# Kernel tuning notes

Hardware: AMD Instinct MI355X
Metric: run time of the kernel (lower is better)

The kernel has to match this reference:

```python
import jax, jax.numpy as jnp
import numpy as np

H = 128

def _gru_cell(x, h, w_ih, w_hh, b_ih, b_hh):
    # PyTorch GRUCell semantics; w_* are [3H, H], gate order r, z, n.
    gi = x @ w_ih.T + b_ih
    gh = h @ w_hh.T + b_hh
    ir, iz, in_ = jnp.split(gi, 3, axis=-1)
    hr, hz, hn = jnp.split(gh, 3, axis=-1)
    r = jax.nn.sigmoid(ir + hr)
    z = jax.nn.sigmoid(iz + hz)
    n = jnp.tanh(in_ + r * hn)
    return (1.0 - z) * n + z * h


def setup_inputs() -> dict:
    key = jax.random.key(0)
    ks = jax.random.split(key, 24)
    s = 0.05
    d = {}
    d["weapon_features"] = jax.random.normal(ks[0], (4, 8, 64, 4), jnp.float32)
    d["target_features"] = jax.random.normal(ks[1], (4, 8, 64, 4), jnp.float32)
    d["edge_features"] = jax.random.uniform(ks[2], (4, 8, 64, 64, 1), jnp.float32)
    # projections (torch Linear convention: weight [out, in])
    d["wp_w"] = jax.random.normal(ks[3], (H, 4), jnp.float32) * s
    d["wp_b"] = jnp.zeros((H,), jnp.float32)
    d["tp_w"] = jax.random.normal(ks[4], (H, 4), jnp.float32) * s
    d["tp_b"] = jnp.zeros((H,), jnp.float32)
    d["ep_w"] = jax.random.normal(ks[5], (H, 1), jnp.float32) * s
    d["ep_b"] = jnp.zeros((H,), jnp.float32)
    # message / edge-update linears [H, 3H]
    d["eu_w"] = jax.random.normal(ks[6], (H, 3 * H), jnp.float32) * s
    d["eu_b"] = jnp.zeros((H,), jnp.float32)
    d["wm_w"] = jax.random.normal(ks[7], (H, 3 * H), jnp.float32) * s
    d["wm_b"] = jnp.zeros((H,), jnp.float32)
    d["tm_w"] = jax.random.normal(ks[8], (H, 3 * H), jnp.float32) * s
    d["tm_b"] = jnp.zeros((H,), jnp.float32)
    # GRU cells
    d["gru_w_ih_w"] = jax.random.normal(ks[9], (3 * H, H), jnp.float32) * s
    d["gru_w_hh_w"] = jax.random.normal(ks[10], (3 * H, H), jnp.float32) * s
    d["gru_b_ih_w"] = jnp.zeros((3 * H,), jnp.float32)
    d["gru_b_hh_w"] = jnp.zeros((3 * H,), jnp.float32)
    d["gru_w_ih_t"] = jax.random.normal(ks[11], (3 * H, H), jnp.float32) * s
    d["gru_w_hh_t"] = jax.random.normal(ks[12], (3 * H, H), jnp.float32) * s
    d["gru_b_ih_t"] = jnp.zeros((3 * H,), jnp.float32)
    d["gru_b_hh_t"] = jnp.zeros((3 * H,), jnp.float32)
    return d


def reference(weapon_features, target_features, edge_features,
              wp_w, wp_b, tp_w, tp_b, ep_w, ep_b,
              eu_w, eu_b, wm_w, wm_b, tm_w, tm_b,
              gru_w_ih_w, gru_w_hh_w, gru_b_ih_w, gru_b_hh_w,
              gru_w_ih_t, gru_w_hh_t, gru_b_ih_t, gru_b_hh_t):
    B, P, W = weapon_features.shape[:3]
    T = target_features.shape[2]
    h = wp_w.shape[0]

    weapon_h = weapon_features @ wp_w.T + wp_b          # [B,P,W,H]
    target_h = target_features @ tp_w.T + tp_b          # [B,P,T,H]
    edge_h = edge_features @ ep_w.T + ep_b              # [B,P,W,T,H]

    # edge_update(cat([w_exp, t_exp, edge_h])) == sum of three slice-linears,
    # broadcast-added; avoids materializing the [B,P,W,T,3H] concat.
    ea, eb, ec = eu_w[:, :h], eu_w[:, h:2 * h], eu_w[:, 2 * h:]
    edge_pre = ((weapon_h @ ea.T)[:, :, :, None, :]
                + (target_h @ eb.T)[:, :, None, :, :]
                + edge_h @ ec.T + eu_b)
    edge_h_new = jnp.tanh(edge_pre)                     # [B,P,W,T,H]

    # weapon_msg(cat([w_exp, t_exp, edge_h_new])).sum(dim=3)
    wa, wb, wc = wm_w[:, :h], wm_w[:, h:2 * h], wm_w[:, 2 * h:]
    weapon_msgs = (T * (weapon_h @ wa.T)
                   + (target_h.sum(axis=2) @ wb.T)[:, :, None, :]
                   + edge_h_new.sum(axis=3) @ wc.T
                   + T * wm_b)                          # [B,P,W,H]

    # target_msg(cat([t_exp, w_exp, edge_h_new])).sum(dim=2)
    ta, tb, tc = tm_w[:, :h], tm_w[:, h:2 * h], tm_w[:, 2 * h:]
    target_msgs = (W * (target_h @ ta.T)
                   + (weapon_h.sum(axis=2) @ tb.T)[:, :, None, :]
                   + edge_h_new.sum(axis=2) @ tc.T
                   + W * tm_b)                          # [B,P,T,H]

    weapon_h_new = _gru_cell(weapon_msgs.reshape(-1, h), weapon_h.reshape(-1, h),
                             gru_w_ih_w, gru_w_hh_w, gru_b_ih_w, gru_b_hh_w)
    weapon_h_new = weapon_h_new.reshape(B, P, W, h)

    target_h_new = _gru_cell(target_msgs.reshape(-1, h), target_h.reshape(-1, h),
                             gru_w_ih_t, gru_w_hh_t, gru_b_ih_t, gru_b_hh_t)
    target_h_new = target_h_new.reshape(B, P, T, h)

    return weapon_h_new, target_h_new, edge_h_new
```

## Files before the change

### kernel.cpp

```cpp
#include <hip/hip_runtime.h>

#define DEV __device__ __forceinline__

constexpr int H  = 128;
constexpr int BP = 32;
constexpr int NR = 2048;

constexpr int WH_OFF    = 0;
constexpr int TH_OFF    = WH_OFF + NR*H;
constexpr int WHS_OFF   = TH_OFF + NR*H;
constexpr int THS_OFF   = WHS_OFF + BP*H;
constexpr int V1_OFF    = THS_OFF + BP*H;
constexpr int C0_OFF    = V1_OFF + H;
constexpr int WT1_OFF   = C0_OFF + H;
constexpr int WT2_OFF   = WT1_OFF + 128*640;
constexpr int WCT_OFF   = WT2_OFF + 128*640;
constexpr int TCT_OFF   = WCT_OFF + 128*128;
constexpr int WIHWT_OFF = TCT_OFF + 128*128;
constexpr int WIHTT_OFF = WIHWT_OFF + 128*384;
constexpr int WBT_OFF   = WIHTT_OFF + 128*384;
constexpr int TBT_OFF   = WBT_OFF + 128*128;
constexpr int OUT1_OFF  = TBT_OFF + 128*128;
constexpr int OUT2_OFF  = OUT1_OFF + NR*640;
constexpr int ESW_OFF   = OUT2_OFF + NR*640;
constexpr int ESTP_OFF  = ESW_OFF + NR*H;
constexpr int MSGW_OFF  = ESTP_OFF + 8*NR*H;
constexpr int MSGT_OFF  = MSGW_OFF + NR*H;
constexpr int GIW_OFF   = MSGT_OFF + NR*H;
constexpr int GIT_OFF   = GIW_OFF + NR*384;
constexpr int WBV_OFF   = GIT_OFF + NR*384;
constexpr int TBV_OFF   = WBV_OFF + BP*H;

DEV float fast_tanh(float x) {
  float e = __builtin_amdgcn_exp2f(x * 2.8853900817779268f);
  return fmaf(-2.0f, __builtin_amdgcn_rcpf(e + 1.0f), 1.0f);
}
DEV float fast_sigmoid(float x) {
  float e = __builtin_amdgcn_exp2f(x * -1.4426950408889634f);
  return __builtin_amdgcn_rcpf(1.0f + e);
}

__global__ __launch_bounds__(256) void k1_proj_transpose(
    const float* __restrict__ wf, const float* __restrict__ tf,
    const float* __restrict__ wp_w, const float* __restrict__ wp_b,
    const float* __restrict__ tp_w, const float* __restrict__ tp_b,
    const float* __restrict__ eu_w, const float* __restrict__ wm_w,
    const float* __restrict__ tm_w,
    const float* __restrict__ whh_w, const float* __restrict__ whh_t,
    const float* __restrict__ wih_w, const float* __restrict__ wih_t,
    float* __restrict__ ws)
{
  int bid = blockIdx.x, tid = threadIdx.x;
  if (bid < 2048) {
    int gid = bid*256 + tid;
    int m = gid >> 7;
    int j = gid & 127;
    int side = m >> 11;
    int n = m & 2047;
    const float* F  = side ? tf : wf;
    const float* Pw = side ? tp_w : wp_w;
    const float* Pb = side ? tp_b : wp_b;
    float4 x  = *(const float4*)&F[n*4];
    float4 wv = *(const float4*)&Pw[j*4];
    float v = x.x*wv.x + x.y*wv.y + x.z*wv.z + x.w*wv.w + Pb[j];
    ws[(side ? TH_OFF : WH_OFF) + n*H + j] = v;
  } else {
    int idx = (bid - 2048)*256 + tid;
    if (idx < 131072) {
      int which = idx >> 14;
      int r = idx & 16383;
      int k = r >> 7, j = r & 127;
      float v; float* dst;
      switch (which) {
        case 0: v = eu_w[j*384 + k];        dst = ws + WT1_OFF + k*640 + j;       break;
        case 1: v = wm_w[j*384 + k];        dst = ws + WT1_OFF + k*640 + 128 + j; break;
        case 2: v = eu_w[j*384 + 128 + k];  dst = ws + WT2_OFF + k*640 + j;       break;
        case 3: v = tm_w[j*384 + k];        dst = ws + WT2_OFF + k*640 + 128 + j; break;
        case 4: v = wm_w[j*384 + 256 + k];  dst = ws + WCT_OFF + k*128 + j;       break;
        case 5: v = tm_w[j*384 + 256 + k];  dst = ws + TCT_OFF + k*128 + j;       break;
        case 6: v = wm_w[j*384 + 128 + k];  dst = ws + WBT_OFF + k*128 + j;       break;
        default:v = tm_w[j*384 + 128 + k];  dst = ws + TBT_OFF + k*128 + j;       break;
      }
      *dst = v;
    } else {
      int idx2 = idx - 131072;
      int which = idx2 / 49152;
      int r = idx2 % 49152;
      int k = r / 384, j = r % 384;
      float v; float* dst;
      switch (which) {
        case 0: v = whh_w[j*128 + k]; dst = ws + WT1_OFF + k*640 + 256 + j; break;
        case 1: v = whh_t[j*128 + k]; dst = ws + WT2_OFF + k*640 + 256 + j; break;
        case 2: v = wih_w[j*128 + k]; dst = ws + WIHWT_OFF + k*384 + j;     break;
        default:v = wih_t[j*128 + k]; dst = ws + WIHTT_OFF + k*384 + j;     break;
      }
      *dst = v;
    }
  }
}

__global__ __launch_bounds__(256) void k2_sums(
    float* __restrict__ ws,
    const float* __restrict__ ep_w, const float* __restrict__ ep_b,
    const float* __restrict__ eu_w, const float* __restrict__ eu_b)
{
  int bid = blockIdx.x, tid = threadIdx.x;
  if (bid < 32) {
    int j = tid & 127, half = tid >> 7;
    const float* src = ws + (half ? TH_OFF : WH_OFF) + bid*64*H + j;
    float s = 0.f;
    #pragma unroll 8
    for (int t = 0; t < 64; ++t) s += src[t*H];
    ws[(half ? THS_OFF : WHS_OFF) + bid*H + j] = s;
  } else if (tid < 128) {
    int j = tid;
    float s1 = 0.f, s0 = 0.f;
    for (int k = 0; k < 128; ++k) {
      float ec = eu_w[j*384 + 256 + k];
      s1 = fmaf(ec, ep_w[k], s1);
      s0 = fmaf(ec, ep_b[k], s0);
    }
    ws[V1_OFF + j] = s1;
    ws[C0_OFF + j] = s0 + eu_b[j];
  }
}

#define FMA4(A, s, Wv) do { A.x = fmaf(s, Wv.x, A.x); A.y = fmaf(s, Wv.y, A.y); \
                            A.z = fmaf(s, Wv.z, A.z); A.w = fmaf(s, Wv.w, A.w); } while (0)

DEV void stage_x_direct(float* Xs, const float* __restrict__ X, int row0, int tid) {
  const float* src = X + row0*128;
  #pragma unroll
  for (int q = 0; q < 4; ++q) {
    int idx = q*1024 + tid*4;
    *(float4*)&Xs[idx] = *(const float4*)&src[idx];
  }
}

DEV void stage_x_sum8(float* Xs, const float* __restrict__ base, int row0, int tid) {
  #pragma unroll
  for (int q = 0; q < 4; ++q) {
    int idx = q*1024 + tid*4;
    float4 s = *(const float4*)&base[row0*128 + idx];
    #pragma unroll
    for (int wt = 1; wt < 8; ++wt) {
      float4 v = *(const float4*)&base[wt*(NR*H) + row0*128 + idx];
      s.x += v.x; s.y += v.y; s.z += v.z; s.w += v.w;
    }
    *(float4*)&Xs[idx] = s;
  }
}

DEV void gemm_core(const float* __restrict__ Wt, int ldw, int j0,
                   const float* Xs, float* Ws, int tid, float4 acc[4])
{
  const int tc = tid & 31, tr = tid >> 5;
  const int jj = tc*4, r0 = tr*4;
  #pragma unroll
  for (int i = 0; i < 4; ++i) acc[i] = make_float4(0.f, 0.f, 0.f, 0.f);
  for (int kc = 0; kc < 128; kc += 32) {
    __syncthreads();
    #pragma unroll
    for (int q = 0; q < 4; ++q) {
      int idx = q*1024 + tid*4;
      int kk = idx >> 7, j = idx & 127;
      *(float4*)&Ws[idx] = *(const float4*)&Wt[(kc+kk)*ldw + j0 + j];
    }
    __syncthreads();
    #pragma unroll
    for (int kk = 0; kk < 32; kk += 4) {
      float4 w0 = *(const float4*)&Ws[(kk+0)*128 + jj];
      float4 w1 = *(const float4*)&Ws[(kk+1)*128 + jj];
      float4 w2 = *(const float4*)&Ws[(kk+2)*128 + jj];
      float4 w3 = *(const float4*)&Ws[(kk+3)*128 + jj];
      #pragma unroll
      for (int rr = 0; rr < 4; ++rr) {
        float4 xq = *(const float4*)&Xs[(r0+rr)*128 + kc + kk];
        FMA4(acc[rr], xq.x, w0);
        FMA4(acc[rr], xq.y, w1);
        FMA4(acc[rr], xq.z, w2);
        FMA4(acc[rr], xq.w, w3);
      }
    }
  }
}

__global__ __launch_bounds__(256) void k3_gemm1(float* __restrict__ ws)
{
  __shared__ float Xs[32*128];
  __shared__ float Wsh[32*128];
  int bid = blockIdx.x, tid = threadIdx.x;
  const int tc = tid & 31, tr = tid >> 5;
  const int jj = tc*4, r0 = tr*4;
  float4 acc[4];
  if (bid < 640) {
    int side = bid >= 320;
    int b2 = bid - (side ? 320 : 0);
    int rt = b2 & 63, ct = b2 >> 6;
    int row0 = rt*32;
    stage_x_direct(Xs, ws + (side ? TH_OFF : WH_OFF), row0, tid);
    gemm_core(ws + (side ? WT2_OFF : WT1_OFF), 640, ct*128, Xs, Wsh, tid, acc);
    float* C = ws + (side ? OUT2_OFF : OUT1_OFF);
    #pragma unroll
    for (int rr = 0; rr < 4; ++rr)
      *(float4*)&C[(row0+r0+rr)*640 + ct*128 + jj] = acc[rr];
  } else {
    int which = bid - 640;
    stage_x_direct(Xs, ws + (which ? WHS_OFF : THS_OFF), 0, tid);
    gemm_core(ws + (which ? TBT_OFF : WBT_OFF), 128, 0, Xs, Wsh, tid, acc);
    float* C = ws + (which ? TBV_OFF : WBV_OFF);
    #pragma unroll
    for (int rr = 0; rr < 4; ++rr)
      *(float4*)&C[(r0+rr)*128 + jj] = acc[rr];
  }
}

__global__ __launch_bounds__(256) void k4_edge(
    const float* __restrict__ ef, float* __restrict__ ws, float* __restrict__ out)
{
  __shared__ float e_lds[8*64];
  __shared__ float red[2][8][128];
  int bid = blockIdx.x, tid = threadIdx.x;
  int bp = bid >> 3, wt = bid & 7;
  int j = tid & 127, tsel = tid >> 7;
  float v1j = ws[V1_OFF + j], c0j = ws[C0_OFF + j];
  {
    const float* esrc = ef + bp*4096 + wt*512;
    *(float2*)&e_lds[tid*2] = *(const float2*)&esrc[tid*2];
  }
  float a_reg[8];
  #pragma unroll
  for (int w = 0; w < 8; ++w)
    a_reg[w] = ws[OUT1_OFF + (bp*64 + wt*8 + w)*640 + j];
  __syncthreads();
  float tsum[8] = {0,0,0,0,0,0,0,0};
  float* edst = out + 524288 + (bp*64 + wt*8)*64*128;
  const float* btp = ws + OUT2_OFF + bp*64*640 + j;
  float* pdst = ws + ESTP_OFF + wt*(NR*H) + bp*64*128 + j;
  for (int i = 0; i < 32; ++i) {
    int t = 2*i + tsel;
    float base = btp[t*640] + c0j;
    float wsum = 0.f;
    #pragma unroll
    for (int w = 0; w < 8; ++w) {
      float ev = e_lds[w*64 + t];
      float pre = a_reg[w] + fmaf(ev, v1j, base);
      float hv = fast_tanh(pre);
      edst[(w*64 + t)*128 + j] = hv;
      tsum[w] += hv;
      wsum += hv;
    }
    pdst[t*128] = wsum;
  }
  #pragma unroll
  for (int w = 0; w < 8; ++w) red[tsel][w][j] = tsum[w];
  __syncthreads();
  if (tsel == 0) {
    #pragma unroll
    for (int w = 0; w < 8; ++w)
      ws[ESW_OFF + (bp*64 + wt*8 + w)*128 + j] = red[0][w][j] + red[1][w][j];
  }
}

__global__ __launch_bounds__(256) void k5_gemm2(
    float* __restrict__ ws, const float* __restrict__ wm_b, const float* __restrict__ tm_b)
{
  __shared__ float Xs[32*128];
  __shared__ float Wsh[32*128];
  int bid = blockIdx.x, tid = threadIdx.x;
  int side = bid >> 6, rt = bid & 63;
  int row0 = rt*32;
  const int tc = tid & 31, tr = tid >> 5;
  const int jj = tc*4, r0 = tr*4;
  if (side == 0) stage_x_direct(Xs, ws + ESW_OFF, row0, tid);
  else           stage_x_sum8(Xs, ws + ESTP_OFF, row0, tid);
  float4 acc[4];
  gemm_core(ws + (side ? TCT_OFF : WCT_OFF), 128, 0, Xs, Wsh, tid, acc);
  const float* OUTx = ws + (side ? OUT2_OFF : OUT1_OFF);
  const float* BV   = ws + (side ? TBV_OFF : WBV_OFF);
  const float* mb   = side ? tm_b : wm_b;
  float* MSG        = ws + (side ? MSGT_OFF : MSGW_OFF);
  float4 b4 = *(const float4*)&mb[jj];
  #pragma unroll
  for (int rr = 0; rr < 4; ++rr) {
    int n = row0 + r0 + rr;
    float4 wa4 = *(const float4*)&OUTx[n*640 + 128 + jj];
    float4 bv4 = *(const float4*)&BV[(n >> 6)*128 + jj];
    float4 r;
    r.x = acc[rr].x + 64.f*wa4.x + bv4.x + 64.f*b4.x;
    r.y = acc[rr].y + 64.f*wa4.y + bv4.y + 64.f*b4.y;
    r.z = acc[rr].z + 64.f*wa4.z + bv4.z + 64.f*b4.z;
    r.w = acc[rr].w + 64.f*wa4.w + bv4.w + 64.f*b4.w;
    *(float4*)&MSG[n*128 + jj] = r;
  }
}

__global__ __launch_bounds__(256) void k6_gemm3(float* __restrict__ ws)
{
  __shared__ float Xs[32*128];
  __shared__ float Wsh[32*128];
  int bid = blockIdx.x, tid = threadIdx.x;
  int side = bid >= 192;
  int b2 = bid - (side ? 192 : 0);
  int rt = b2 & 63, ct = b2 >> 6;
  int row0 = rt*32;
  const int tc = tid & 31, tr = tid >> 5;
  const int jj = tc*4, r0 = tr*4;
  stage_x_direct(Xs, ws + (side ? MSGT_OFF : MSGW_OFF), row0, tid);
  float4 acc[4];
  gemm_core(ws + (side ? WIHTT_OFF : WIHWT_OFF), 384, ct*128, Xs, Wsh, tid, acc);
  float* C = ws + (side ? GIT_OFF : GIW_OFF);
  #pragma unroll
  for (int rr = 0; rr < 4; ++rr)
    *(float4*)&C[(row0+r0+rr)*384 + ct*128 + jj] = acc[rr];
}

__global__ __launch_bounds__(256) void k7_gru(
    const float* __restrict__ ws, float* __restrict__ out,
    const float* __restrict__ bih_w, const float* __restrict__ bhh_w,
    const float* __restrict__ bih_t, const float* __restrict__ bhh_t)
{
  int gid = blockIdx.x*256 + threadIdx.x;
  int m = gid >> 7, j = gid & 127;
  int side = m >> 11, n = m & 2047;
  const float* GI = ws + (side ? GIT_OFF : GIW_OFF) + n*384;
  const float* GH = ws + (side ? OUT2_OFF : OUT1_OFF) + n*640 + 256;
  const float* Hv = ws + (side ? TH_OFF : WH_OFF) + n*128;
  const float* bi = side ? bih_t : bih_w;
  const float* bh = side ? bhh_t : bhh_w;
  float gir = GI[j]       + bi[j];
  float giz = GI[128 + j] + bi[128 + j];
  float gin = GI[256 + j] + bi[256 + j];
  float ghr = GH[j]       + bh[j];
  float ghz = GH[128 + j] + bh[128 + j];
  float ghn = GH[256 + j] + bh[256 + j];
  float r  = fast_sigmoid(gir + ghr);
  float z  = fast_sigmoid(giz + ghz);
  float nn = fast_tanh(gin + r*ghn);
  float h  = Hv[j];
  out[side*262144 + n*128 + j] = (1.f - z)*nn + z*h;
}

extern "C" void kernel_launch(void* const* d_in, const int* in_sizes, int n_in,
                              void* d_out, int out_size, void* d_ws, size_t ws_size,
                              hipStream_t stream)
{
  const float* wf    = (const float*)d_in[0];
  const float* tf    = (const float*)d_in[1];
  const float* ef    = (const float*)d_in[2];
  const float* wp_w  = (const float*)d_in[3];
  const float* wp_b  = (const float*)d_in[4];
  const float* tp_w  = (const float*)d_in[5];
  const float* tp_b  = (const float*)d_in[6];
  const float* ep_w  = (const float*)d_in[7];
  const float* ep_b  = (const float*)d_in[8];
  const float* eu_w  = (const float*)d_in[9];
  const float* eu_b  = (const float*)d_in[10];
  const float* wm_w  = (const float*)d_in[11];
  const float* wm_b  = (const float*)d_in[12];
  const float* tm_w  = (const float*)d_in[13];
  const float* tm_b  = (const float*)d_in[14];
  const float* wih_w = (const float*)d_in[15];
  const float* whh_w = (const float*)d_in[16];
  const float* bih_w = (const float*)d_in[17];
  const float* bhh_w = (const float*)d_in[18];
  const float* wih_t = (const float*)d_in[19];
  const float* whh_t = (const float*)d_in[20];
  const float* bih_t = (const float*)d_in[21];
  const float* bhh_t = (const float*)d_in[22];
  float* ws  = (float*)d_ws;
  float* out = (float*)d_out;

  hipLaunchKernelGGL(k1_proj_transpose, dim3(3328), dim3(256), 0, stream,
                     wf, tf, wp_w, wp_b, tp_w, tp_b, eu_w, wm_w, tm_w,
                     whh_w, whh_t, wih_w, wih_t, ws);
  hipLaunchKernelGGL(k2_sums,  dim3(33),   dim3(256), 0, stream, ws, ep_w, ep_b, eu_w, eu_b);
  hipLaunchKernelGGL(k3_gemm1, dim3(642),  dim3(256), 0, stream, ws);
  hipLaunchKernelGGL(k4_edge,  dim3(256),  dim3(256), 0, stream, ef, ws, out);
  hipLaunchKernelGGL(k5_gemm2, dim3(128),  dim3(256), 0, stream, ws, wm_b, tm_b);
  hipLaunchKernelGGL(k6_gemm3, dim3(384),  dim3(256), 0, stream, ws);
  hipLaunchKernelGGL(k7_gru,   dim3(2048), dim3(256), 0, stream, ws, out,
                     bih_w, bhh_w, bih_t, bhh_t);
}
```

Before: 188.7 us.

## Split weight transpose into LDS-tiled kernel, fuse sums into projection, widen edge grid

Weight transposes move into a separate LDS-tiled kernel (20 blocks) so that global reads and writes are coalesced. The per-batch hidden sums are now computed directly from raw features in the projection kernel, which removes the k2 launch. The edge kernel splits the weapon dimension four ways instead of eight per block, doubling the grid. It stages the target projection in LDS and writes edge outputs with nontemporal stores. The price is a 16-way partial-sum buffer that k5 must reduce, plus more LDS use per edge block.

```diff
diff --git a/kernel.cpp b/kernel.cpp
--- a/kernel.cpp
+++ b/kernel.cpp
@@ -24,7 +24,7 @@
 constexpr int OUT2_OFF  = OUT1_OFF + NR*640;
 constexpr int ESW_OFF   = OUT2_OFF + NR*640;
 constexpr int ESTP_OFF  = ESW_OFF + NR*H;
-constexpr int MSGW_OFF  = ESTP_OFF + 8*NR*H;
+constexpr int MSGW_OFF  = ESTP_OFF + 16*NR*H;
 constexpr int MSGT_OFF  = MSGW_OFF + NR*H;
 constexpr int GIW_OFF   = MSGT_OFF + NR*H;
 constexpr int GIT_OFF   = GIW_OFF + NR*384;
@@ -40,16 +40,62 @@
   return __builtin_amdgcn_rcpf(1.0f + e);
 }
 
-__global__ __launch_bounds__(256) void k1_proj_transpose(
-    const float* __restrict__ wf, const float* __restrict__ tf,
-    const float* __restrict__ wp_w, const float* __restrict__ wp_b,
-    const float* __restrict__ tp_w, const float* __restrict__ tp_b,
+__global__ __launch_bounds__(256) void k0_transpose(
     const float* __restrict__ eu_w, const float* __restrict__ wm_w,
     const float* __restrict__ tm_w,
     const float* __restrict__ whh_w, const float* __restrict__ whh_t,
     const float* __restrict__ wih_w, const float* __restrict__ wih_t,
     float* __restrict__ ws)
 {
+  __shared__ float T[128*133];
+  int tt = blockIdx.x, tid = threadIdx.x;
+  const float* src; int rs = 384, co = 0, row0 = 0, dsto, ldd, j0;
+  switch (tt) {
+    case 0:  src=eu_w;  dsto=WT1_OFF; ldd=640; j0=0;   break;
+    case 1:  src=wm_w;  dsto=WT1_OFF; ldd=640; j0=128; break;
+    case 2: case 3: case 4:
+      src=whh_w; rs=128; row0=(tt-2)*128; dsto=WT1_OFF; ldd=640; j0=256+(tt-2)*128; break;
+    case 5:  src=eu_w;  co=128; dsto=WT2_OFF; ldd=640; j0=0; break;
+    case 6:  src=tm_w;  dsto=WT2_OFF; ldd=640; j0=128; break;
+    case 7: case 8: case 9:
+      src=whh_t; rs=128; row0=(tt-7)*128; dsto=WT2_OFF; ldd=640; j0=256+(tt-7)*128; break;
+    case 10: src=wm_w; co=256; dsto=WCT_OFF; ldd=128; j0=0; break;
+    case 11: src=tm_w; co=256; dsto=TCT_OFF; ldd=128; j0=0; break;
+    case 12: src=wm_w; co=128; dsto=WBT_OFF; ldd=128; j0=0; break;
+    case 13: src=tm_w; co=128; dsto=TBT_OFF; ldd=128; j0=0; break;
+    case 14: case 15: case 16:
+      src=wih_w; rs=128; row0=(tt-14)*128; dsto=WIHWT_OFF; ldd=384; j0=(tt-14)*128; break;
+    default:
+      src=wih_t; rs=128; row0=(tt-17)*128; dsto=WIHTT_OFF; ldd=384; j0=(tt-17)*128; break;
+  }
+  #pragma unroll
+  for (int q = 0; q < 16; ++q) {
+    int idx = q*1024 + tid*4;
+    int r = idx >> 7, c = idx & 127;
+    float4 v = *(const float4*)&src[(row0 + r)*rs + co + c];
+    float* t = &T[r*133 + c];
+    t[0]=v.x; t[1]=v.y; t[2]=v.z; t[3]=v.w;
+  }
+  __syncthreads();
+  float* dst = ws + dsto;
+  #pragma unroll
+  for (int q = 0; q < 64; ++q) {
+    int idx = q*256 + tid;
+    int k = idx >> 7, j = idx & 127;
+    dst[k*ldd + j0 + j] = T[j*133 + k];
+  }
+}
+
+__global__ __launch_bounds__(256) void k1_proj(
+    const float* __restrict__ wf, const float* __restrict__ tf,
+    const float* __restrict__ wp_w, const float* __restrict__ wp_b,
+    const float* __restrict__ tp_w, const float* __restrict__ tp_b,
+    const float* __restrict__ eu_w,
+    const float* __restrict__ ep_w, const float* __restrict__ ep_b,
+    const float* __restrict__ eu_b,
+    float* __restrict__ ws)
+{
+  __shared__ float fs[2][32][4];
   int bid = blockIdx.x, tid = threadIdx.x;
   if (bid < 2048) {
     int gid = bid*256 + tid;
@@ -65,63 +111,40 @@
     float v = x.x*wv.x + x.y*wv.y + x.z*wv.z + x.w*wv.w + Pb[j];
     ws[(side ? TH_OFF : WH_OFF) + n*H + j] = v;
   } else {
-    int idx = (bid - 2048)*256 + tid;
-    if (idx < 131072) {
-      int which = idx >> 14;
-      int r = idx & 16383;
-      int k = r >> 7, j = r & 127;
-      float v; float* dst;
-      switch (which) {
-        case 0: v = eu_w[j*384 + k];        dst = ws + WT1_OFF + k*640 + j;       break;
-        case 1: v = wm_w[j*384 + k];        dst = ws + WT1_OFF + k*640 + 128 + j; break;
-        case 2: v = eu_w[j*384 + 128 + k];  dst = ws + WT2_OFF + k*640 + j;       break;
-        case 3: v = tm_w[j*384 + k];        dst = ws + WT2_OFF + k*640 + 128 + j; break;
-        case 4: v = wm_w[j*384 + 256 + k];  dst = ws + WCT_OFF + k*128 + j;       break;
-        case 5: v = tm_w[j*384 + 256 + k];  dst = ws + TCT_OFF + k*128 + j;       break;
-        case 6: v = wm_w[j*384 + 128 + k];  dst = ws + WBT_OFF + k*128 + j;       break;
-        default:v = tm_w[j*384 + 128 + k];  dst = ws + TBT_OFF + k*128 + j;       break;
+    {
+      int side = tid >> 7, r = tid & 127;
+      int bp = r >> 2, c = r & 3;
+      const float* F = side ? tf : wf;
+      float s = 0.f;
+      #pragma unroll 8
+      for (int w = 0; w < 64; ++w) s += F[bp*256 + w*4 + c];
+      fs[side][bp][c] = s;
+    }
+    __syncthreads();
+    {
+      int side = tid >> 7, j = tid & 127;
+      const float* Pw = side ? tp_w : wp_w;
+      const float* Pb = side ? tp_b : wp_b;
+      float4 wv = *(const float4*)&Pw[j*4];
+      float pb = Pb[j] * 64.f;
+      float* dst = ws + (side ? THS_OFF : WHS_OFF) + j;
+      #pragma unroll 4
+      for (int bp = 0; bp < 32; ++bp) {
+        float4 f = *(const float4*)&fs[side][bp][0];
+        dst[bp*128] = f.x*wv.x + f.y*wv.y + f.z*wv.z + f.w*wv.w + pb;
       }
-      *dst = v;
-    } else {
-      int idx2 = idx - 131072;
-      int which = idx2 / 49152;
-      int r = idx2 % 49152;
-      int k = r / 384, j = r % 384;
-      float v; float* dst;
-      switch (which) {
-        case 0: v = whh_w[j*128 + k]; dst = ws + WT1_OFF + k*640 + 256 + j; break;
-        case 1: v = whh_t[j*128 + k]; dst = ws + WT2_OFF + k*640 + 256 + j; break;
-        case 2: v = wih_w[j*128 + k]; dst = ws + WIHWT_OFF + k*384 + j;     break;
-        default:v = wih_t[j*128 + k]; dst = ws + WIHTT_OFF + k*384 + j;     break;
+    }
+    if (tid < 128) {
+      int j = tid;
+      float s1 = 0.f, s0 = 0.f;
+      for (int k = 0; k < 128; ++k) {
+        float ec = eu_w[j*384 + 256 + k];
+        s1 = fmaf(ec, ep_w[k], s1);
+        s0 = fmaf(ec, ep_b[k], s0);
       }
-      *dst = v;
-    }
-  }
-}
-
-__global__ __launch_bounds__(256) void k2_sums(
-    float* __restrict__ ws,
-    const float* __restrict__ ep_w, const float* __restrict__ ep_b,
-    const float* __restrict__ eu_w, const float* __restrict__ eu_b)
-{
-  int bid = blockIdx.x, tid = threadIdx.x;
-  if (bid < 32) {
-    int j = tid & 127, half = tid >> 7;
-    const float* src = ws + (half ? TH_OFF : WH_OFF) + bid*64*H + j;
-    float s = 0.f;
-    #pragma unroll 8
-    for (int t = 0; t < 64; ++t) s += src[t*H];
-    ws[(half ? THS_OFF : WHS_OFF) + bid*H + j] = s;
-  } else if (tid < 128) {
-    int j = tid;
-    float s1 = 0.f, s0 = 0.f;
-    for (int k = 0; k < 128; ++k) {
-      float ec = eu_w[j*384 + 256 + k];
-      s1 = fmaf(ec, ep_w[k], s1);
-      s0 = fmaf(ec, ep_b[k], s0);
-    }
-    ws[V1_OFF + j] = s1;
-    ws[C0_OFF + j] = s0 + eu_b[j];
+      ws[V1_OFF + j] = s1;
+      ws[C0_OFF + j] = s0 + eu_b[j];
+    }
   }
 }
 
@@ -137,13 +160,13 @@
   }
 }
 
-DEV void stage_x_sum8(float* Xs, const float* __restrict__ base, int row0, int tid) {
+DEV void stage_x_sum16(float* Xs, const float* __restrict__ base, int row0, int tid) {
   #pragma unroll
   for (int q = 0; q < 4; ++q) {
     int idx = q*1024 + tid*4;
     float4 s = *(const float4*)&base[row0*128 + idx];
     #pragma unroll
-    for (int wt = 1; wt < 8; ++wt) {
+    for (int wt = 1; wt < 16; ++wt) {
       float4 v = *(const float4*)&base[wt*(NR*H) + row0*128 + idx];
       s.x += v.x; s.y += v.y; s.z += v.z; s.w += v.w;
     }
@@ -218,47 +241,56 @@
 __global__ __launch_bounds__(256) void k4_edge(
     const float* __restrict__ ef, float* __restrict__ ws, float* __restrict__ out)
 {
-  __shared__ float e_lds[8*64];
-  __shared__ float red[2][8][128];
+  __shared__ float Bs[64*128];
+  __shared__ float e_lds[4*64];
+  __shared__ float red[2][4][128];
   int bid = blockIdx.x, tid = threadIdx.x;
-  int bp = bid >> 3, wt = bid & 7;
+  int bp = bid >> 4, wq = bid & 15;
   int j = tid & 127, tsel = tid >> 7;
   float v1j = ws[V1_OFF + j], c0j = ws[C0_OFF + j];
   {
-    const float* esrc = ef + bp*4096 + wt*512;
-    *(float2*)&e_lds[tid*2] = *(const float2*)&esrc[tid*2];
-  }
-  float a_reg[8];
-  #pragma unroll
-  for (int w = 0; w < 8; ++w)
-    a_reg[w] = ws[OUT1_OFF + (bp*64 + wt*8 + w)*640 + j];
+    const float* o2 = ws + OUT2_OFF + bp*64*640;
+    #pragma unroll
+    for (int q = 0; q < 8; ++q) {
+      int idx = q*256 + tid;
+      int t = idx >> 5, jq = (idx & 31)*4;
+      *(float4*)&Bs[t*128 + jq] = *(const float4*)&o2[t*640 + jq];
+    }
+  }
+  if (tid < 64) {
+    int w = tid >> 4, t4 = (tid & 15)*4;
+    *(float4*)&e_lds[w*64 + t4] = *(const float4*)&ef[bp*4096 + (wq*4 + w)*64 + t4];
+  }
+  float a_reg[4];
+  #pragma unroll
+  for (int w = 0; w < 4; ++w)
+    a_reg[w] = ws[OUT1_OFF + (bp*64 + wq*4 + w)*640 + j];
   __syncthreads();
-  float tsum[8] = {0,0,0,0,0,0,0,0};
-  float* edst = out + 524288 + (bp*64 + wt*8)*64*128;
-  const float* btp = ws + OUT2_OFF + bp*64*640 + j;
-  float* pdst = ws + ESTP_OFF + wt*(NR*H) + bp*64*128 + j;
+  float tsum[4] = {0.f, 0.f, 0.f, 0.f};
+  float* edst = out + 524288 + (bp*64 + wq*4)*8192 + j;
+  float* pdst = ws + ESTP_OFF + wq*(NR*H) + bp*64*128 + j;
   for (int i = 0; i < 32; ++i) {
     int t = 2*i + tsel;
-    float base = btp[t*640] + c0j;
+    float base = Bs[t*128 + j] + c0j;
     float wsum = 0.f;
     #pragma unroll
-    for (int w = 0; w < 8; ++w) {
+    for (int w = 0; w < 4; ++w) {
       float ev = e_lds[w*64 + t];
       float pre = a_reg[w] + fmaf(ev, v1j, base);
       float hv = fast_tanh(pre);
-      edst[(w*64 + t)*128 + j] = hv;
+      __builtin_nontemporal_store(hv, &edst[w*8192 + t*128]);
       tsum[w] += hv;
       wsum += hv;
     }
     pdst[t*128] = wsum;
   }
   #pragma unroll
-  for (int w = 0; w < 8; ++w) red[tsel][w][j] = tsum[w];
+  for (int w = 0; w < 4; ++w) red[tsel][w][j] = tsum[w];
   __syncthreads();
   if (tsel == 0) {
     #pragma unroll
-    for (int w = 0; w < 8; ++w)
-      ws[ESW_OFF + (bp*64 + wt*8 + w)*128 + j] = red[0][w][j] + red[1][w][j];
+    for (int w = 0; w < 4; ++w)
+      ws[ESW_OFF + (bp*64 + wq*4 + w)*128 + j] = red[0][w][j] + red[1][w][j];
   }
 }
 
@@ -273,7 +305,7 @@
   const int tc = tid & 31, tr = tid >> 5;
   const int jj = tc*4, r0 = tr*4;
   if (side == 0) stage_x_direct(Xs, ws + ESW_OFF, row0, tid);
-  else           stage_x_sum8(Xs, ws + ESTP_OFF, row0, tid);
+  else           stage_x_sum16(Xs, ws + ESTP_OFF, row0, tid);
   float4 acc[4];
   gemm_core(ws + (side ? TCT_OFF : WCT_OFF), 128, 0, Xs, Wsh, tid, acc);
   const float* OUTx = ws + (side ? OUT2_OFF : OUT1_OFF);
@@ -287,10 +319,10 @@
     float4 wa4 = *(const float4*)&OUTx[n*640 + 128 + jj];
     float4 bv4 = *(const float4*)&BV[(n >> 6)*128 + jj];
     float4 r;
-    r.x = acc[rr].x + 64.f*wa4.x + bv4.x + 64.f*b4.x;
-    r.y = acc[rr].y + 64.f*wa4.y + bv4.y + 64.f*b4.y;
-    r.z = acc[rr].z + 64.f*wa4.z + bv4.z + 64.f*b4.z;
-    r.w = acc[rr].w + 64.f*wa4.w + bv4.w + 64.f*b4.w;
+    r.x = acc[rr].x + 64.f*(wa4.x + b4.x) + bv4.x;
+    r.y = acc[rr].y + 64.f*(wa4.y + b4.y) + bv4.y;
+    r.z = acc[rr].z + 64.f*(wa4.z + b4.z) + bv4.z;
+    r.w = acc[rr].w + 64.f*(wa4.w + b4.w) + bv4.w;
     *(float4*)&MSG[n*128 + jj] = r;
   }
 }
@@ -371,12 +403,12 @@
   float* ws  = (float*)d_ws;
   float* out = (float*)d_out;
 
-  hipLaunchKernelGGL(k1_proj_transpose, dim3(3328), dim3(256), 0, stream,
-                     wf, tf, wp_w, wp_b, tp_w, tp_b, eu_w, wm_w, tm_w,
-                     whh_w, whh_t, wih_w, wih_t, ws);
-  hipLaunchKernelGGL(k2_sums,  dim3(33),   dim3(256), 0, stream, ws, ep_w, ep_b, eu_w, eu_b);
+  hipLaunchKernelGGL(k0_transpose, dim3(20), dim3(256), 0, stream,
+                     eu_w, wm_w, tm_w, whh_w, whh_t, wih_w, wih_t, ws);
+  hipLaunchKernelGGL(k1_proj, dim3(2049), dim3(256), 0, stream,
+                     wf, tf, wp_w, wp_b, tp_w, tp_b, eu_w, ep_w, ep_b, eu_b, ws);
   hipLaunchKernelGGL(k3_gemm1, dim3(642),  dim3(256), 0, stream, ws);
-  hipLaunchKernelGGL(k4_edge,  dim3(256),  dim3(256), 0, stream, ef, ws, out);
+  hipLaunchKernelGGL(k4_edge,  dim3(512),  dim3(256), 0, stream, ef, ws, out);
   hipLaunchKernelGGL(k5_gemm2, dim3(128),  dim3(256), 0, stream, ws, wm_b, tm_b);
   hipLaunchKernelGGL(k6_gemm3, dim3(384),  dim3(256), 0, stream, ws);
   hipLaunchKernelGGL(k7_gru,   dim3(2048), dim3(256), 0, stream, ws, out,
```

New measurement: 189.2 us. About the same (+0.3%).
